# Performance work log

Hardware: AMD Instinct MI355X
Metric: run time of the kernel (lower is better)

The kernel has to match this reference:

```python
import jax, jax.numpy as jnp
import numpy as np

NUM_CLASSES = 1000
DENSE_DIM = 64 * 64  # 4096, hardcoded in the module
BATCH = 8192
W0, W1 = 0.5, 0.5  # self.weights


def setup_inputs() -> dict:
    key = jax.random.key(0)
    k1, k2, k3, k4 = jax.random.split(key, 4)
    logits = jax.random.normal(k1, (BATCH, NUM_CLASSES), dtype=jnp.float32)
    dense_out = jax.random.normal(k2, (BATCH, DENSE_DIM), dtype=jnp.float32)
    target = jax.random.randint(k3, (BATCH,), 0, NUM_CLASSES, dtype=jnp.int32)
    # dense_labels buffer: random 0/1 per (class, dense) cell, as in __init__
    dense_labels = jax.random.bernoulli(k4, 0.5, (NUM_CLASSES, DENSE_DIM)).astype(jnp.float32)
    return {"logits": logits, "dense_out": dense_out, "target": target,
            "dense_labels": dense_labels}


def _bce_with_logits_mean(x, y):
    # numerically stable BCEWithLogitsLoss (mean reduction)
    return jnp.mean(jnp.maximum(x, 0.0) - x * y + jnp.log1p(jnp.exp(-jnp.abs(x))))


def reference(logits, dense_out, target, dense_labels):
    # --- accumulation (detached in the original; side-effect state) ---
    probs = jax.lax.stop_gradient(jax.nn.sigmoid(dense_out))  # [B, D]
    dense_output_sum = jax.ops.segment_sum(probs, target, num_segments=NUM_CLASSES)  # [C, D]
    total_accumulated = jax.ops.segment_sum(
        jnp.ones((BATCH,), dtype=jnp.float32), target, num_segments=NUM_CLASSES)  # [C]

    # --- losses ---
    dense_target = dense_labels[target]  # per-sample gather of label rows [B, D]
    logp = jax.nn.log_softmax(logits, axis=-1)
    loss1 = -jnp.mean(jnp.take_along_axis(logp, target[:, None], axis=1))  # CrossEntropyLoss
    loss2 = _bce_with_logits_mean(dense_out, dense_target)
    loss = loss1 * W0 + loss2 * W1
    return loss, dense_output_sum, total_accumulated
```

## Files before the change

kernel.cpp:

```cpp
#include <hip/hip_runtime.h>
#include <math.h>

#define NC   1000
#define DD   4096
#define BB   8192

#define MAIN_BLOCKS (NC * 4)
#define CE_BLOCKS   (BB / 4)
#define TOT_BLOCKS  (MAIN_BLOCKS + CE_BLOCKS)
#define MAXN 144
#define NSLOT 32


#define ACC1(xv, yv, acc)                                                     \
    {                                                                         \
        float e = __expf(-fabsf(xv));                                         \
        float inv = __builtin_amdgcn_rcpf(1.f + e);                           \
        acc += (xv >= 0.f) ? inv : e * inv;                                   \
        bce += fmaxf(xv, 0.f) - xv * yv + __logf(1.f + e);                    \
    }

#define ACC1W(xv, yv, acc, w)                                                 \
    {                                                                         \
        float e = __expf(-fabsf(xv));                                         \
        float inv = __builtin_amdgcn_rcpf(1.f + e);                           \
        float sg = (xv >= 0.f) ? inv : e * inv;                               \
        float tm = fmaxf(xv, 0.f) - xv * yv + __logf(1.f + e);                \
        acc += w * sg;                                                        \
        bce += w * tm;                                                        \
    }

__global__ __launch_bounds__(256, 4) void fused_k(const float* __restrict__ logits,
                                                  const float* __restrict__ dense_out,
                                                  const int*   __restrict__ target,
                                                  const float* __restrict__ dense_labels,
                                                  float* __restrict__ out,
                                                  double* __restrict__ loss1,
                                                  double* __restrict__ loss2) {
    int bx = blockIdx.x;
    int t  = threadIdx.x;
    int wave = t >> 6;
    int lane = t & 63;

    __shared__ int   sidx[MAXN];
    __shared__ int   s_n;
    __shared__ float red[4];

    if (bx < MAIN_BLOCKS) {
        int c     = bx >> 2;
        int chunk = bx & 3;
        int d     = chunk * 1024 + (t << 2);

        if (t == 0) s_n = 0;
        __syncthreads();

        const float4* dp4 = (const float4*)(dense_out + d);
        float4 y = *(const float4*)(dense_labels + (size_t)c * DD + d);

        const int4* tp = (const int4*)target;
        #pragma unroll
        for (int k = 0; k < 8; ++k) {
            int4 v = tp[k * 256 + t];
            int s0 = (k * 256 + t) * 4;
            if (v.x == c) { int p = atomicAdd(&s_n, 1); sidx[p] = s0;     }
            if (v.y == c) { int p = atomicAdd(&s_n, 1); sidx[p] = s0 + 1; }
            if (v.z == c) { int p = atomicAdd(&s_n, 1); sidx[p] = s0 + 2; }
            if (v.w == c) { int p = atomicAdd(&s_n, 1); sidx[p] = s0 + 3; }
        }
        __syncthreads();
        int n  = s_n;
        int n8 = (n + 7) & ~7;
        if (t < n8 - n) sidx[n + t] = sidx[0];
        __syncthreads();

        float a0 = 0.f, a1 = 0.f, a2 = 0.f, a3 = 0.f, bce = 0.f;

        for (int base = 0; base < n8; base += 8) {
            float4 xa[8];
            #pragma unroll
            for (int j = 0; j < 8; ++j)
                xa[j] = dp4[sidx[base + j] * (DD / 4)];

            if (base + 8 <= n) {
                #pragma unroll
                for (int j = 0; j < 8; ++j) {
                    ACC1(xa[j].x, y.x, a0) ACC1(xa[j].y, y.y, a1)
                    ACC1(xa[j].z, y.z, a2) ACC1(xa[j].w, y.w, a3)
                }
            } else {
                #pragma unroll
                for (int j = 0; j < 8; ++j) {
                    float w = (base + j < n) ? 1.f : 0.f;
                    ACC1W(xa[j].x, y.x, a0, w) ACC1W(xa[j].y, y.y, a1, w)
                    ACC1W(xa[j].z, y.z, a2, w) ACC1W(xa[j].w, y.w, a3, w)
                }
            }
        }

        float* p = out + 1 + (size_t)c * DD + d;
        p[0] = a0; p[1] = a1; p[2] = a2; p[3] = a3;

        if (chunk == 0 && t == 0) out[1 + (size_t)NC * DD + c] = (float)n;

        #pragma unroll
        for (int o2 = 32; o2 > 0; o2 >>= 1) bce += __shfl_xor(bce, o2);
        if (lane == 0) red[wave] = bce;
        __syncthreads();
        if (t == 0)
            atomicAdd(&loss2[bx & (NSLOT - 1)],
                      (double)(red[0] + red[1] + red[2] + red[3]));
    } else {
        int i = (bx - MAIN_BLOCKS) * 4 + wave;
        const float* row = logits + (size_t)i * NC;
        int j0 = lane * 4;

        float4 r0 = *(const float4*)(row + j0);
        float4 r1 = *(const float4*)(row + j0 + 256);
        float4 r2 = *(const float4*)(row + j0 + 512);
        float4 r3;
        if (j0 + 768 < NC) r3 = *(const float4*)(row + j0 + 768);
        else r3 = make_float4(-INFINITY, -INFINITY, -INFINITY, -INFINITY);
        float tl = row[target[i]];

        float mx = fmaxf(fmaxf(fmaxf(r0.x, r0.y), fmaxf(r0.z, r0.w)),
                         fmaxf(fmaxf(r1.x, r1.y), fmaxf(r1.z, r1.w)));
        mx = fmaxf(mx, fmaxf(fmaxf(r2.x, r2.y), fmaxf(r2.z, r2.w)));
        mx = fmaxf(mx, fmaxf(fmaxf(r3.x, r3.y), fmaxf(r3.z, r3.w)));
        #pragma unroll
        for (int o = 32; o > 0; o >>= 1) mx = fmaxf(mx, __shfl_xor(mx, o));

        float s = __expf(r0.x - mx) + __expf(r0.y - mx) + __expf(r0.z - mx) + __expf(r0.w - mx)
                + __expf(r1.x - mx) + __expf(r1.y - mx) + __expf(r1.z - mx) + __expf(r1.w - mx)
                + __expf(r2.x - mx) + __expf(r2.y - mx) + __expf(r2.z - mx) + __expf(r2.w - mx)
                + __expf(r3.x - mx) + __expf(r3.y - mx) + __expf(r3.z - mx) + __expf(r3.w - mx);
        #pragma unroll
        for (int o = 32; o > 0; o >>= 1) s += __shfl_xor(s, o);

        if (lane == 0) red[wave] = -(tl - mx - __logf(s));
        __syncthreads();
        if (t == 0)
            atomicAdd(&loss1[bx & (NSLOT - 1)],
                      (double)(red[0] + red[1] + red[2] + red[3]));
    }
}

__global__ void fin_k(const double* __restrict__ loss1,
                      const double* __restrict__ loss2,
                      float* __restrict__ out) {
    double l1 = 0.0, l2 = 0.0;
    #pragma unroll
    for (int i = 0; i < NSLOT; ++i) { l1 += loss1[i]; l2 += loss2[i]; }
    out[0] = (float)(0.5 * (l1 / (double)BB) +
                     0.5 * (l2 / ((double)BB * (double)DD)));
}

extern "C" void kernel_launch(void* const* d_in, const int* in_sizes, int n_in,
                              void* d_out, int out_size, void* d_ws, size_t ws_size,
                              hipStream_t stream) {
    const float* logits       = (const float*)d_in[0];
    const float* dense_out    = (const float*)d_in[1];
    const int*   target       = (const int*)d_in[2];
    const float* dense_labels = (const float*)d_in[3];
    float* out = (float*)d_out;

    char* ws = (char*)d_ws;
    double* loss1 = (double*)(ws + 0);
    double* loss2 = (double*)(ws + 256);

    hipMemsetAsync(d_ws, 0, 512, stream);

    fused_k<<<TOT_BLOCKS, 256, 0, stream>>>(logits, dense_out, target,
                                            dense_labels, out, loss1, loss2);
    fin_k<<<1, 1, 0, stream>>>(loss1, loss2, out);
}
```

Measured before the change: 243.6 us.

## Split fused kernel into separate dense and CE kernels, shrink gather batch, use log2

Splits the combined kernel into a dense-loss kernel and a separate cross-entropy kernel, launched back to back on the same stream. The gather loop now loads 4 rows per iteration instead of 8, which lowers register pressure. The BCE log term is accumulated with log2 in a separate sum and scaled by ln2 once at the end. The split removes the block-index branch but adds a kernel launch and serialises the CE work after the dense work, where before the two could overlap.

```diff
diff --git a/kernel.cpp b/kernel.cpp
--- a/kernel.cpp
+++ b/kernel.cpp
@@ -7,9 +7,9 @@
 
 #define MAIN_BLOCKS (NC * 4)
 #define CE_BLOCKS   (BB / 4)
-#define TOT_BLOCKS  (MAIN_BLOCKS + CE_BLOCKS)
 #define MAXN 144
 #define NSLOT 32
+#define LN2  0.69314718055994531f
 
 
 #define ACC1(xv, yv, acc)                                                     \
@@ -17,7 +17,8 @@
         float e = __expf(-fabsf(xv));                                         \
         float inv = __builtin_amdgcn_rcpf(1.f + e);                           \
         acc += (xv >= 0.f) ? inv : e * inv;                                   \
-        bce += fmaxf(xv, 0.f) - xv * yv + __logf(1.f + e);                    \
+        bceA += fmaxf(xv, 0.f) - xv * yv;                                     \
+        bceB += __log2f(1.f + e);                                             \
     }
 
 #define ACC1W(xv, yv, acc, w)                                                 \
@@ -25,18 +26,16 @@
         float e = __expf(-fabsf(xv));                                         \
         float inv = __builtin_amdgcn_rcpf(1.f + e);                           \
         float sg = (xv >= 0.f) ? inv : e * inv;                               \
-        float tm = fmaxf(xv, 0.f) - xv * yv + __logf(1.f + e);                \
         acc += w * sg;                                                        \
-        bce += w * tm;                                                        \
+        bceA += w * (fmaxf(xv, 0.f) - xv * yv);                               \
+        bceB += w * __log2f(1.f + e);                                         \
     }
 
-__global__ __launch_bounds__(256, 4) void fused_k(const float* __restrict__ logits,
-                                                  const float* __restrict__ dense_out,
-                                                  const int*   __restrict__ target,
-                                                  const float* __restrict__ dense_labels,
-                                                  float* __restrict__ out,
-                                                  double* __restrict__ loss1,
-                                                  double* __restrict__ loss2) {
+__global__ __launch_bounds__(256, 4) void main_k(const float* __restrict__ dense_out,
+                                                 const int*   __restrict__ target,
+                                                 const float* __restrict__ dense_labels,
+                                                 float* __restrict__ out,
+                                                 double* __restrict__ loss2) {
     int bx = blockIdx.x;
     int t  = threadIdx.x;
     int wave = t >> 6;
@@ -46,102 +45,112 @@
     __shared__ int   s_n;
     __shared__ float red[4];
 
-    if (bx < MAIN_BLOCKS) {
-        int c     = bx >> 2;
-        int chunk = bx & 3;
-        int d     = chunk * 1024 + (t << 2);
+    int c     = bx >> 2;
+    int chunk = bx & 3;
+    int d     = chunk * 1024 + (t << 2);
 
-        if (t == 0) s_n = 0;
-        __syncthreads();
+    if (t == 0) s_n = 0;
+    __syncthreads();
 
-        const float4* dp4 = (const float4*)(dense_out + d);
-        float4 y = *(const float4*)(dense_labels + (size_t)c * DD + d);
+    const float4* dp4 = (const float4*)(dense_out + d);
+    float4 y = *(const float4*)(dense_labels + (size_t)c * DD + d);
 
-        const int4* tp = (const int4*)target;
+    const int4* tp = (const int4*)target;
+    #pragma unroll
+    for (int k = 0; k < 8; ++k) {
+        int4 v = tp[k * 256 + t];
+        int s0 = (k * 256 + t) * 4;
+        if (v.x == c) { int p = atomicAdd(&s_n, 1); sidx[p] = s0;     }
+        if (v.y == c) { int p = atomicAdd(&s_n, 1); sidx[p] = s0 + 1; }
+        if (v.z == c) { int p = atomicAdd(&s_n, 1); sidx[p] = s0 + 2; }
+        if (v.w == c) { int p = atomicAdd(&s_n, 1); sidx[p] = s0 + 3; }
+    }
+    __syncthreads();
+    int n  = s_n;
+    int n4 = (n + 3) & ~3;
+    if (t < n4 - n) sidx[n + t] = sidx[0];
+    __syncthreads();
+
+    float a0 = 0.f, a1 = 0.f, a2 = 0.f, a3 = 0.f, bceA = 0.f, bceB = 0.f;
+
+    for (int base = 0; base < n4; base += 4) {
+        float4 xa[4];
         #pragma unroll
-        for (int k = 0; k < 8; ++k) {
-            int4 v = tp[k * 256 + t];
-            int s0 = (k * 256 + t) * 4;
-            if (v.x == c) { int p = atomicAdd(&s_n, 1); sidx[p] = s0;     }
-            if (v.y == c) { int p = atomicAdd(&s_n, 1); sidx[p] = s0 + 1; }
-            if (v.z == c) { int p = atomicAdd(&s_n, 1); sidx[p] = s0 + 2; }
-            if (v.w == c) { int p = atomicAdd(&s_n, 1); sidx[p] = s0 + 3; }
-        }
-        __syncthreads();
-        int n  = s_n;
-        int n8 = (n + 7) & ~7;
-        if (t < n8 - n) sidx[n + t] = sidx[0];
-        __syncthreads();
+        for (int j = 0; j < 4; ++j)
+            xa[j] = dp4[sidx[base + j] * (DD / 4)];
 
-        float a0 = 0.f, a1 = 0.f, a2 = 0.f, a3 = 0.f, bce = 0.f;
-
-        for (int base = 0; base < n8; base += 8) {
-            float4 xa[8];
+        if (base + 4 <= n) {
             #pragma unroll
-            for (int j = 0; j < 8; ++j)
-                xa[j] = dp4[sidx[base + j] * (DD / 4)];
-
-            if (base + 8 <= n) {
-                #pragma unroll
-                for (int j = 0; j < 8; ++j) {
-                    ACC1(xa[j].x, y.x, a0) ACC1(xa[j].y, y.y, a1)
-                    ACC1(xa[j].z, y.z, a2) ACC1(xa[j].w, y.w, a3)
-                }
-            } else {
-                #pragma unroll
-                for (int j = 0; j < 8; ++j) {
-                    float w = (base + j < n) ? 1.f : 0.f;
-                    ACC1W(xa[j].x, y.x, a0, w) ACC1W(xa[j].y, y.y, a1, w)
-                    ACC1W(xa[j].z, y.z, a2, w) ACC1W(xa[j].w, y.w, a3, w)
-                }
+            for (int j = 0; j < 4; ++j) {
+                ACC1(xa[j].x, y.x, a0) ACC1(xa[j].y, y.y, a1)
+                ACC1(xa[j].z, y.z, a2) ACC1(xa[j].w, y.w, a3)
+            }
+        } else {
+            #pragma unroll
+            for (int j = 0; j < 4; ++j) {
+                float w = (base + j < n) ? 1.f : 0.f;
+                ACC1W(xa[j].x, y.x, a0, w) ACC1W(xa[j].y, y.y, a1, w)
+                ACC1W(xa[j].z, y.z, a2, w) ACC1W(xa[j].w, y.w, a3, w)
             }
         }
+    }
 
-        float* p = out + 1 + (size_t)c * DD + d;
-        p[0] = a0; p[1] = a1; p[2] = a2; p[3] = a3;
+    float* p = out + 1 + (size_t)c * DD + d;
+    p[0] = a0; p[1] = a1; p[2] = a2; p[3] = a3;
 
-        if (chunk == 0 && t == 0) out[1 + (size_t)NC * DD + c] = (float)n;
+    if (chunk == 0 && t == 0) out[1 + (size_t)NC * DD + c] = (float)n;
 
-        #pragma unroll
-        for (int o2 = 32; o2 > 0; o2 >>= 1) bce += __shfl_xor(bce, o2);
-        if (lane == 0) red[wave] = bce;
-        __syncthreads();
-        if (t == 0)
-            atomicAdd(&loss2[bx & (NSLOT - 1)],
-                      (double)(red[0] + red[1] + red[2] + red[3]));
-    } else {
-        int i = (bx - MAIN_BLOCKS) * 4 + wave;
-        const float* row = logits + (size_t)i * NC;
-        int j0 = lane * 4;
+    float bce = bceA + LN2 * bceB;
+    #pragma unroll
+    for (int o2 = 32; o2 > 0; o2 >>= 1) bce += __shfl_xor(bce, o2);
+    if (lane == 0) red[wave] = bce;
+    __syncthreads();
+    if (t == 0)
+        atomicAdd(&loss2[bx & (NSLOT - 1)],
+                  (double)(red[0] + red[1] + red[2] + red[3]));
+}
 
-        float4 r0 = *(const float4*)(row + j0);
-        float4 r1 = *(const float4*)(row + j0 + 256);
-        float4 r2 = *(const float4*)(row + j0 + 512);
-        float4 r3;
-        if (j0 + 768 < NC) r3 = *(const float4*)(row + j0 + 768);
-        else r3 = make_float4(-INFINITY, -INFINITY, -INFINITY, -INFINITY);
-        float tl = row[target[i]];
+__global__ __launch_bounds__(256) void ce_k(const float* __restrict__ logits,
+                                            const int*   __restrict__ target,
+                                            double* __restrict__ loss1) {
+    int bx = blockIdx.x;
+    int t  = threadIdx.x;
+    int wave = t >> 6;
+    int lane = t & 63;
 
-        float mx = fmaxf(fmaxf(fmaxf(r0.x, r0.y), fmaxf(r0.z, r0.w)),
-                         fmaxf(fmaxf(r1.x, r1.y), fmaxf(r1.z, r1.w)));
-        mx = fmaxf(mx, fmaxf(fmaxf(r2.x, r2.y), fmaxf(r2.z, r2.w)));
-        mx = fmaxf(mx, fmaxf(fmaxf(r3.x, r3.y), fmaxf(r3.z, r3.w)));
-        #pragma unroll
-        for (int o = 32; o > 0; o >>= 1) mx = fmaxf(mx, __shfl_xor(mx, o));
+    __shared__ float red[4];
 
-        float s = __expf(r0.x - mx) + __expf(r0.y - mx) + __expf(r0.z - mx) + __expf(r0.w - mx)
-                + __expf(r1.x - mx) + __expf(r1.y - mx) + __expf(r1.z - mx) + __expf(r1.w - mx)
-                + __expf(r2.x - mx) + __expf(r2.y - mx) + __expf(r2.z - mx) + __expf(r2.w - mx)
-                + __expf(r3.x - mx) + __expf(r3.y - mx) + __expf(r3.z - mx) + __expf(r3.w - mx);
-        #pragma unroll
-        for (int o = 32; o > 0; o >>= 1) s += __shfl_xor(s, o);
+    int i = bx * 4 + wave;
+    const float* row = logits + (size_t)i * NC;
+    int j0 = lane * 4;
 
-        if (lane == 0) red[wave] = -(tl - mx - __logf(s));
-        __syncthreads();
-        if (t == 0)
-            atomicAdd(&loss1[bx & (NSLOT - 1)],
-                      (double)(red[0] + red[1] + red[2] + red[3]));
-    }
+    float4 r0 = *(const float4*)(row + j0);
+    float4 r1 = *(const float4*)(row + j0 + 256);
+    float4 r2 = *(const float4*)(row + j0 + 512);
+    float4 r3;
+    if (j0 + 768 < NC) r3 = *(const float4*)(row + j0 + 768);
+    else r3 = make_float4(-INFINITY, -INFINITY, -INFINITY, -INFINITY);
+    float tl = row[target[i]];
+
+    float mx = fmaxf(fmaxf(fmaxf(r0.x, r0.y), fmaxf(r0.z, r0.w)),
+                     fmaxf(fmaxf(r1.x, r1.y), fmaxf(r1.z, r1.w)));
+    mx = fmaxf(mx, fmaxf(fmaxf(r2.x, r2.y), fmaxf(r2.z, r2.w)));
+    mx = fmaxf(mx, fmaxf(fmaxf(r3.x, r3.y), fmaxf(r3.z, r3.w)));
+    #pragma unroll
+    for (int o = 32; o > 0; o >>= 1) mx = fmaxf(mx, __shfl_xor(mx, o));
+
+    float s = __expf(r0.x - mx) + __expf(r0.y - mx) + __expf(r0.z - mx) + __expf(r0.w - mx)
+            + __expf(r1.x - mx) + __expf(r1.y - mx) + __expf(r1.z - mx) + __expf(r1.w - mx)
+            + __expf(r2.x - mx) + __expf(r2.y - mx) + __expf(r2.z - mx) + __expf(r2.w - mx)
+            + __expf(r3.x - mx) + __expf(r3.y - mx) + __expf(r3.z - mx) + __expf(r3.w - mx);
+    #pragma unroll
+    for (int o = 32; o > 0; o >>= 1) s += __shfl_xor(s, o);
+
+    if (lane == 0) red[wave] = -(tl - mx - __logf(s));
+    __syncthreads();
+    if (t == 0)
+        atomicAdd(&loss1[bx & (NSLOT - 1)],
+                  (double)(red[0] + red[1] + red[2] + red[3]));
 }
 
 __global__ void fin_k(const double* __restrict__ loss1,
@@ -169,7 +178,8 @@
 
     hipMemsetAsync(d_ws, 0, 512, stream);
 
-    fused_k<<<TOT_BLOCKS, 256, 0, stream>>>(logits, dense_out, target,
-                                            dense_labels, out, loss1, loss2);
+    main_k<<<MAIN_BLOCKS, 256, 0, stream>>>(dense_out, target, dense_labels,
+                                            out, loss2);
+    ce_k<<<CE_BLOCKS, 256, 0, stream>>>(logits, target, loss1);
     fin_k<<<1, 1, 0, stream>>>(loss1, loss2, out);
 }
```

Measured after the change: 256.0 us. 1.05x slower.
